# Kernel optimization log

Measured on AMD Instinct MI355X. Metric: run time of the kernel, lower is better.

## Reference

```python
import jax, jax.numpy as jnp
import numpy as np

FEATURE_SIZE = 10 * 64 * 64  # 40960
HIDDEN1 = 512
HIDDEN2 = 256
BATCH = 4096


def setup_inputs() -> dict:
    key = jax.random.key(0)
    ks = jax.random.split(key, 8)
    # Sparse binary-ish features emulated as dense uniform (math is identical).
    white_features = jax.random.uniform(ks[0], (BATCH, FEATURE_SIZE), dtype=jnp.float32)
    black_features = jax.random.uniform(ks[1], (BATCH, FEATURE_SIZE), dtype=jnp.float32)
    s_ft = 1.0 / np.sqrt(FEATURE_SIZE)
    s_fc1 = 1.0 / np.sqrt(HIDDEN1 * 2)
    s_fc2 = 1.0 / np.sqrt(HIDDEN2)
    ft_w = jax.random.uniform(ks[2], (HIDDEN1, FEATURE_SIZE), minval=-s_ft, maxval=s_ft, dtype=jnp.float32)
    ft_b = jax.random.uniform(ks[3], (HIDDEN1,), minval=-s_ft, maxval=s_ft, dtype=jnp.float32)
    fc1_w = jax.random.uniform(ks[4], (HIDDEN2, HIDDEN1 * 2), minval=-s_fc1, maxval=s_fc1, dtype=jnp.float32)
    fc1_b = jax.random.uniform(ks[5], (HIDDEN2,), minval=-s_fc1, maxval=s_fc1, dtype=jnp.float32)
    fc2_w = jax.random.uniform(ks[6], (1, HIDDEN2), minval=-s_fc2, maxval=s_fc2, dtype=jnp.float32)
    fc2_b = jax.random.uniform(ks[7], (1,), minval=-s_fc2, maxval=s_fc2, dtype=jnp.float32)
    return dict(white_features=white_features, black_features=black_features,
                ft_w=ft_w, ft_b=ft_b, fc1_w=fc1_w, fc1_b=fc1_b, fc2_w=fc2_w, fc2_b=fc2_b)


def reference(white_features, black_features, ft_w, ft_b, fc1_w, fc1_b, fc2_w, fc2_b):
    # Feature transform per perspective, clamped to [0, 1]
    white_ft = jnp.clip(white_features @ ft_w.T + ft_b, 0.0, 1.0)  # [B, H1]
    black_ft = jnp.clip(black_features @ ft_w.T + ft_b, 0.0, 1.0)  # [B, H1]
    combined = jnp.concatenate([white_ft, black_ft], axis=1)       # [B, 2*H1]
    x = jax.nn.relu(combined @ fc1_w.T + fc1_b)                    # [B, H2]
    x = x @ fc2_w.T + fc2_b                                        # [B, 1]
    return x.squeeze(-1)
```

## Files before the change

kernel.cpp:

```cpp
#include <hip/hip_runtime.h>
#include <stdint.h>

#define BATCH 4096
#define FEAT  40960
#define H1    512
#define KS    4
#define KCHUNK (FEAT / KS)
#define NSTEPS (KCHUNK / 32)
#define NTILES (FEAT / 32)
#define WTILE  32768

typedef float f32x4 __attribute__((ext_vector_type(4)));
typedef short s16x8 __attribute__((ext_vector_type(8)));
typedef unsigned int u32x2 __attribute__((ext_vector_type(2)));
typedef unsigned int u32x4 __attribute__((ext_vector_type(4)));

__device__ __forceinline__ unsigned bfpack2(float lo, float hi) {
  unsigned a = __float_as_uint(lo);
  unsigned b = __float_as_uint(hi);
  a += 0x7FFFu + ((a >> 16) & 1u);
  b += 0x7FFFu + ((b >> 16) & 1u);
  return (a >> 16) | (b & 0xFFFF0000u);
}

__device__ __forceinline__ int lds_swz(int r, int cb) {
  return (r << 6) + (cb ^ (((r >> 1) & 3) << 4));
}

__global__ __launch_bounds__(512)
void wcvt_kernel(const float* __restrict__ ftw, char* __restrict__ wbf) {
  const int T = blockIdx.x;
  const int tid = threadIdx.x;
  const int c  = tid & 7;
  const int r0 = tid >> 3;
#pragma unroll
  for (int pass = 0; pass < 8; ++pass) {
    const int r = pass * 64 + r0;
    const float* src = ftw + (size_t)r * FEAT + T * 32 + c * 4;
    f32x4 v = *(const f32x4*)src;
    u32x2 o;
    o.x = bfpack2(v.x, v.y);
    o.y = bfpack2(v.z, v.w);
    const int nb = r >> 6, f = (r >> 4) & 3, lr = r & 15;
    const int l = (c >> 1) * 16 + lr;
    *(u32x2*)(wbf + (size_t)T * WTILE + ((nb * 4 + f) << 10) + l * 16 +
              (c & 1) * 8) = o;
  }
}

__global__ __launch_bounds__(512, 4)
void ft_gemm_kernel(const float* __restrict__ whiteF,
                    const float* __restrict__ blackF,
                    const char* __restrict__ wbf,
                    float* __restrict__ Ppart) {
  __shared__ char smem[8192];

  const int tid = threadIdx.x, bid = blockIdx.x;
  const int wgid = (bid & 7) * 64 + (bid >> 3);
  const int ks = wgid >> 7;
  const int p  = (wgid >> 6) & 1;
  const int mt = wgid & 63;

  const float* Ag =
      (p == 0 ? whiteF : blackF) + (size_t)(mt * 64) * FEAT + ks * KCHUNK;

  const int a_row = tid >> 3, a_kc = tid & 7;
  const float* aptr = Ag + (size_t)a_row * FEAT + a_kc * 4;
  const int awoff = lds_swz(a_row, a_kc * 8);

  const int lane = tid & 63, wave = tid >> 6;
  const int lrow = lane & 15, lkb = (lane >> 4) * 16;

  const char* wsrc =
      wbf + (size_t)ks * NSTEPS * WTILE + (wave << 12) + lane * 16;

  int a_off[4];
#pragma unroll
  for (int m = 0; m < 4; ++m) a_off[m] = lds_swz(m * 16 + lrow, lkb);

  f32x4 acc[4][4];
#pragma unroll
  for (int m = 0; m < 4; ++m)
#pragma unroll
    for (int n = 0; n < 4; ++n) acc[m][n] = (f32x4){0.f, 0.f, 0.f, 0.f};

  f32x4 raA;
  u32x4 rb[2][4];

  raA = *(const f32x4*)aptr;
#pragma unroll
  for (int n = 0; n < 4; ++n)
    rb[0][n] = *(const u32x4*)(wsrc + (n << 10));

#define GSTEP(B, LAST, t)                                                     \
  {                                                                           \
                    \
    u32x2 av;                                                                 \
    av.x = bfpack2(raA.x, raA.y);                                             \
    av.y = bfpack2(raA.z, raA.w);                                             \
    *(u32x2*)(smem + (B) * 4096 + awoff) = av;                                \
    if (!(LAST)) {    \
      raA = *(const f32x4*)(aptr + (size_t)((t) + 1) * 32);                   \
                                             \
      const char* wsp = wsrc + (size_t)((t) + 1) * WTILE;                     \
      _Pragma("unroll") for (int n = 0; n < 4; ++n)                           \
          rb[(B) ^ 1][n] = *(const u32x4*)(wsp + (n << 10));                  \
    }                                                                         \
    asm volatile("s_waitcnt lgkmcnt(0)" ::: "memory");   \
    __builtin_amdgcn_sched_barrier(0);                                        \
    __builtin_amdgcn_s_barrier();                                             \
    __builtin_amdgcn_sched_barrier(0);                                        \
    const char* base = smem + (B) * 4096;                                     \
    s16x8 af[4];                                                              \
    _Pragma("unroll") for (int m = 0; m < 4; ++m)                             \
        af[m] = *(const s16x8*)(base + a_off[m]);                             \
    _Pragma("unroll") for (int n = 0; n < 4; ++n) {                           \
      s16x8 bfn = __builtin_bit_cast(s16x8, rb[B][n]);                        \
      _Pragma("unroll") for (int m = 0; m < 4; ++m)                           \
          acc[m][n] = __builtin_amdgcn_mfma_f32_16x16x32_bf16(                \
              af[m], bfn, acc[m][n], 0, 0, 0);                                \
    }                                                                         \
  }

  for (int tt = 0; tt < NSTEPS - 2; tt += 2) {
    GSTEP(0, false, tt);
    GSTEP(1, false, tt + 1);
  }
  GSTEP(0, false, NSTEPS - 2);
  GSTEP(1, true, NSTEPS - 1);
#undef GSTEP

  float* Pp = Ppart + ((size_t)(ks * 2 + p) * BATCH + mt * 64) * H1;
  const int r0 = (lane >> 4) * 4;
  const int c0 = wave * 64 + lrow;
#pragma unroll
  for (int m = 0; m < 4; ++m)
#pragma unroll
    for (int n = 0; n < 4; ++n) {
      float* dst = Pp + (size_t)(r0 + m * 16) * H1 + c0 + n * 16;
#pragma unroll
      for (int j = 0; j < 4; ++j) dst[(size_t)j * H1] = acc[m][n][j];
    }
}

__global__ __launch_bounds__(256)
void ft_reduce_kernel(const float* __restrict__ Ppart,
                      const float* __restrict__ ftb,
                      unsigned short* __restrict__ comb) {
  const size_t gid = (size_t)blockIdx.x * 256 + threadIdx.x;
  const int    pp  = (int)(gid / (BATCH * H1 / 4));
  const size_t rem = gid % (BATCH * H1 / 4);
  const int    row = (int)(rem / (H1 / 4));
  const int    n4  = (int)(rem % (H1 / 4)) * 4;

  f32x4 s = (f32x4){0.f, 0.f, 0.f, 0.f};
#pragma unroll
  for (int ks = 0; ks < KS; ++ks)
    s += *(const f32x4*)(Ppart + ((size_t)(ks * 2 + pp) * BATCH + row) * H1 + n4);
  const f32x4 bv = *(const f32x4*)(ftb + n4);
  s += bv;
  s.x = fminf(fmaxf(s.x, 0.f), 1.f);
  s.y = fminf(fmaxf(s.y, 0.f), 1.f);
  s.z = fminf(fmaxf(s.z, 0.f), 1.f);
  s.w = fminf(fmaxf(s.w, 0.f), 1.f);

  u32x2 o;
  o.x = bfpack2(s.x, s.y);
  o.y = bfpack2(s.z, s.w);
  *(u32x2*)(comb + (size_t)row * 1024 + pp * H1 + n4) = o;
}

__global__ __launch_bounds__(256)
void fc_kernel(const unsigned short* __restrict__ comb,
               const float* __restrict__ w1, const float* __restrict__ b1,
               const float* __restrict__ w2, const float* __restrict__ b2,
               float* __restrict__ out) {
  __shared__ char smem[40960];
  __shared__ float rowsum[64];

  const int tid = threadIdx.x;
  const int bm  = blockIdx.x;
  if (tid < 64) rowsum[tid] = 0.f;

  const int a_row = tid >> 2, a_kq = tid & 3;
  const unsigned short* aptr = comb + (size_t)(bm * 64 + a_row) * 1024 + a_kq * 8;
  const float* wptr = w1 + (size_t)a_row * 1024 + a_kq * 8;

  u32x4 raA;
  f32x4 rw0[4], rw1[4];
  auto issue = [&](int t) {
    raA = *(const u32x4*)(aptr + t * 32);
    const float* wp = wptr + t * 32;
#pragma unroll
    for (int s = 0; s < 4; ++s) {
      rw0[s] = *(const f32x4*)(wp + (size_t)s * 64 * 1024);
      rw1[s] = *(const f32x4*)(wp + (size_t)s * 64 * 1024 + 4);
    }
  };

  const int aoff_w = lds_swz(a_row, a_kq * 16);
  int woff_w[4];
#pragma unroll
  for (int s = 0; s < 4; ++s)
    woff_w[s] = 4096 + lds_swz(s * 64 + a_row, a_kq * 16);

  auto cvtwrite = [&](int b) {
    char* base = smem + b * 20480;
    *(u32x4*)(base + aoff_w) = raA;
#pragma unroll
    for (int s = 0; s < 4; ++s) {
      u32x4 wv;
      wv.x = bfpack2(rw0[s].x, rw0[s].y); wv.y = bfpack2(rw0[s].z, rw0[s].w);
      wv.z = bfpack2(rw1[s].x, rw1[s].y); wv.w = bfpack2(rw1[s].z, rw1[s].w);
      *(u32x4*)(base + woff_w[s]) = wv;
    }
  };

  const int lane = tid & 63, wn = tid >> 6;
  const int lrow = lane & 15, lkb = (lane >> 4) * 16;
  int a_off[4], b_off[4];
#pragma unroll
  for (int m = 0; m < 4; ++m) a_off[m] = lds_swz(m * 16 + lrow, lkb);
#pragma unroll
  for (int n = 0; n < 4; ++n) b_off[n] = 4096 + lds_swz(wn * 64 + n * 16 + lrow, lkb);

  f32x4 acc[4][4];
#pragma unroll
  for (int m = 0; m < 4; ++m)
#pragma unroll
    for (int n = 0; n < 4; ++n) acc[m][n] = (f32x4){0.f, 0.f, 0.f, 0.f};

  issue(0);
  for (int t = 0; t < 32; ++t) {
    const int b = t & 1;
    cvtwrite(b);
    if (t + 1 < 32) issue(t + 1);
    asm volatile("s_waitcnt lgkmcnt(0)" ::: "memory");
    __builtin_amdgcn_sched_barrier(0);
    __builtin_amdgcn_s_barrier();
    __builtin_amdgcn_sched_barrier(0);
    char* base = smem + b * 20480;
    s16x8 af[4];
#pragma unroll
    for (int m = 0; m < 4; ++m) af[m] = *(const s16x8*)(base + a_off[m]);
#pragma unroll
    for (int n = 0; n < 4; ++n) {
      s16x8 bfn = *(const s16x8*)(base + b_off[n]);
#pragma unroll
      for (int m = 0; m < 4; ++m)
        acc[m][n] = __builtin_amdgcn_mfma_f32_16x16x32_bf16(af[m], bfn, acc[m][n], 0, 0, 0);
    }
  }

  float b1v[4], w2v[4];
#pragma unroll
  for (int n = 0; n < 4; ++n) {
    const int col = wn * 64 + n * 16 + lrow;
    b1v[n] = b1[col];
    w2v[n] = w2[col];
  }
#pragma unroll
  for (int m = 0; m < 4; ++m)
#pragma unroll
    for (int j = 0; j < 4; ++j) {
      float v = 0.f;
#pragma unroll
      for (int n = 0; n < 4; ++n) {
        float x = acc[m][n][j] + b1v[n];
        x = fmaxf(x, 0.f);
        v += x * w2v[n];
      }
#pragma unroll
      for (int d = 1; d < 16; d <<= 1) v += __shfl_xor(v, d, 64);
      if ((lane & 15) == 0)
        atomicAdd(&rowsum[m * 16 + (lane >> 4) * 4 + j], v);
    }
  __syncthreads();
  if (tid < 64) {
    out[bm * 64 + tid] = rowsum[tid] + b2[0];
  }
}

extern "C" void kernel_launch(void* const* d_in, const int* in_sizes, int n_in,
                              void* d_out, int out_size, void* d_ws, size_t ws_size,
                              hipStream_t stream) {
  const float* whiteF = (const float*)d_in[0];
  const float* blackF = (const float*)d_in[1];
  const float* ftw    = (const float*)d_in[2];
  const float* ftb    = (const float*)d_in[3];
  const float* w1     = (const float*)d_in[4];
  const float* b1     = (const float*)d_in[5];
  const float* w2     = (const float*)d_in[6];
  const float* b2     = (const float*)d_in[7];

  char* wbf = (char*)d_ws;
  const size_t wbf_bytes   = (size_t)NTILES * WTILE;
  const size_t ppart_bytes = (size_t)KS * 2 * BATCH * H1 * sizeof(float);
  float* Ppart = (float*)((char*)d_ws + wbf_bytes);
  unsigned short* comb = (unsigned short*)((char*)d_ws + wbf_bytes + ppart_bytes);
  float* outp = (float*)d_out;

  hipLaunchKernelGGL(wcvt_kernel, dim3(NTILES), dim3(512), 0, stream, ftw, wbf);
  hipLaunchKernelGGL(ft_gemm_kernel, dim3(512), dim3(512), 0, stream,
                     whiteF, blackF, wbf, Ppart);
  hipLaunchKernelGGL(ft_reduce_kernel, dim3((2 * BATCH * H1 / 4) / 256), dim3(256),
                     0, stream, Ppart, ftb, comb);
  hipLaunchKernelGGL(fc_kernel, dim3(BATCH / 64), dim3(256), 0, stream,
                     comb, w1, b1, w2, b2, outp);
}
```

Before: 553.6 us.

## Stream FT weight tiles into LDS via global_load_lds with two-deep prefetch

Weight tiles for the feature-transform GEMM are now copied straight from global memory into double-buffered LDS slots with global_load_lds, instead of being held in registers. Activations are prefetched two steps ahead through vmcnt-based waits. The aim is to free VGPRs and hide global-load latency behind the MFMA work. The LDS footprint grows from 8 KB to 72 KB per 512-thread block, which conflicts with the launch_bounds occupancy hint of 4 blocks and likely cuts resident blocks per CU. The hand-counted vmcnt values also have to match the exact load order.

```diff
diff --git a/kernel.cpp b/kernel.cpp
--- a/kernel.cpp
+++ b/kernel.cpp
@@ -9,6 +9,8 @@
 #define NSTEPS (KCHUNK / 32)
 #define NTILES (FEAT / 32)
 #define WTILE  32768
+#define WSLOT  32768
+#define ALDS   65536
 
 typedef float f32x4 __attribute__((ext_vector_type(4)));
 typedef short s16x8 __attribute__((ext_vector_type(8)));
@@ -25,6 +27,12 @@
 
 __device__ __forceinline__ int lds_swz(int r, int cb) {
   return (r << 6) + (cb ^ (((r >> 1) & 3) << 4));
+}
+
+__device__ __forceinline__ void glds16(const void* g, void* l) {
+  __builtin_amdgcn_global_load_lds(
+      (const __attribute__((address_space(1))) unsigned*)g,
+      (__attribute__((address_space(3))) unsigned*)l, 16, 0, 0);
 }
 
 __global__ __launch_bounds__(512)
@@ -53,7 +61,7 @@
                     const float* __restrict__ blackF,
                     const char* __restrict__ wbf,
                     float* __restrict__ Ppart) {
-  __shared__ char smem[8192];
+  __shared__ char smem[73728];
 
   const int tid = threadIdx.x, bid = blockIdx.x;
   const int wgid = (bid & 7) * 64 + (bid >> 3);
@@ -73,6 +81,7 @@
 
   const char* wsrc =
       wbf + (size_t)ks * NSTEPS * WTILE + (wave << 12) + lane * 16;
+  const int wofs = (wave << 12);
 
   int a_off[4];
 #pragma unroll
@@ -84,51 +93,76 @@
 #pragma unroll
     for (int n = 0; n < 4; ++n) acc[m][n] = (f32x4){0.f, 0.f, 0.f, 0.f};
 
-  f32x4 raA;
-  u32x4 rb[2][4];
-
-  raA = *(const f32x4*)aptr;
-#pragma unroll
-  for (int n = 0; n < 4; ++n)
-    rb[0][n] = *(const u32x4*)(wsrc + (n << 10));
-
-#define GSTEP(B, LAST, t)                                                     \
+  f32x4 raA[2];
+
+  raA[0] = *(const f32x4*)aptr;
+  raA[1] = *(const f32x4*)(aptr + 32);
+#pragma unroll
+  for (int c = 0; c < 4; ++c)
+    glds16(wsrc + c * 1024, smem + 0 * WSLOT + wofs + c * 1024);
+#pragma unroll
+  for (int c = 0; c < 4; ++c)
+    glds16(wsrc + WTILE + c * 1024, smem + 1 * WSLOT + wofs + c * 1024);
+  asm volatile("s_waitcnt vmcnt(9)" ::: "memory");
+  __builtin_amdgcn_sched_barrier(0);
+  {
+    u32x2 av;
+    av.x = bfpack2(raA[0].x, raA[0].y);
+    av.y = bfpack2(raA[0].z, raA[0].w);
+    *(u32x2*)(smem + ALDS + 0 * 4096 + awoff) = av;
+  }
+  raA[0] = *(const f32x4*)(aptr + 2 * 32);
+  asm volatile("s_waitcnt lgkmcnt(0)" ::: "memory");
+  __builtin_amdgcn_sched_barrier(0);
+  __builtin_amdgcn_s_barrier();
+  __builtin_amdgcn_sched_barrier(0);
+
+#define GSTEP(B, t)                                                           \
   {                                                                           \
-                    \
-    u32x2 av;                                                                 \
-    av.x = bfpack2(raA.x, raA.y);                                             \
-    av.y = bfpack2(raA.z, raA.w);                                             \
-    *(u32x2*)(smem + (B) * 4096 + awoff) = av;                                \
-    if (!(LAST)) {    \
-      raA = *(const f32x4*)(aptr + (size_t)((t) + 1) * 32);                   \
-                                             \
-      const char* wsp = wsrc + (size_t)((t) + 1) * WTILE;                     \
-      _Pragma("unroll") for (int n = 0; n < 4; ++n)                           \
-          rb[(B) ^ 1][n] = *(const u32x4*)(wsp + (n << 10));                  \
+    asm volatile("s_waitcnt vmcnt(5)" ::: "memory");   \
+    __builtin_amdgcn_sched_barrier(0);                                        \
+    const char* wbase = smem + (B) * WSLOT + wofs;                            \
+    const char* abase = smem + ALDS + (B) * 4096;                             \
+    s16x8 af[4], wb[4];                                                       \
+    _Pragma("unroll") for (int m = 0; m < 4; ++m)                             \
+        af[m] = *(const s16x8*)(abase + a_off[m]);                            \
+    _Pragma("unroll") for (int n = 0; n < 4; ++n)                             \
+        wb[n] = *(const s16x8*)(wbase + n * 1024 + lane * 16);                \
+    asm volatile("s_waitcnt lgkmcnt(0)" ::: "memory");      \
+    __builtin_amdgcn_sched_barrier(0);                                        \
+    {                     \
+      const int t2 = ((t) + 2 < NSTEPS) ? (t) + 2 : NSTEPS - 1;               \
+      const char* wsp = wsrc + (size_t)t2 * WTILE;                            \
+      char* wdp = smem + (B) * WSLOT + wofs;                                  \
+      _Pragma("unroll") for (int c = 0; c < 4; ++c)                           \
+          glds16(wsp + c * 1024, wdp + c * 1024);                             \
     }                                                                         \
+    {        \
+      u32x2 av;                                                               \
+      av.x = bfpack2(raA[(B) ^ 1].x, raA[(B) ^ 1].y);                         \
+      av.y = bfpack2(raA[(B) ^ 1].z, raA[(B) ^ 1].w);                         \
+      *(u32x2*)(smem + ALDS + ((B) ^ 1) * 4096 + awoff) = av;                 \
+      const int t3 = ((t) + 3 < NSTEPS) ? (t) + 3 : NSTEPS - 1;               \
+      raA[(B) ^ 1] = *(const f32x4*)(aptr + (size_t)t3 * 32);                 \
+    }                                                                         \
+    _Pragma("unroll") for (int n = 0; n < 4; ++n)                             \
+      _Pragma("unroll") for (int m = 0; m < 4; ++m)                           \
+          acc[m][n] = __builtin_amdgcn_mfma_f32_16x16x32_bf16(                \
+              af[m], wb[n], acc[m][n], 0, 0, 0);                              \
     asm volatile("s_waitcnt lgkmcnt(0)" ::: "memory");   \
     __builtin_amdgcn_sched_barrier(0);                                        \
     __builtin_amdgcn_s_barrier();                                             \
     __builtin_amdgcn_sched_barrier(0);                                        \
-    const char* base = smem + (B) * 4096;                                     \
-    s16x8 af[4];                                                              \
-    _Pragma("unroll") for (int m = 0; m < 4; ++m)                             \
-        af[m] = *(const s16x8*)(base + a_off[m]);                             \
-    _Pragma("unroll") for (int n = 0; n < 4; ++n) {                           \
-      s16x8 bfn = __builtin_bit_cast(s16x8, rb[B][n]);                        \
-      _Pragma("unroll") for (int m = 0; m < 4; ++m)                           \
-          acc[m][n] = __builtin_amdgcn_mfma_f32_16x16x32_bf16(                \
-              af[m], bfn, acc[m][n], 0, 0, 0);                                \
-    }                                                                         \
-  }
-
-  for (int tt = 0; tt < NSTEPS - 2; tt += 2) {
-    GSTEP(0, false, tt);
-    GSTEP(1, false, tt + 1);
-  }
-  GSTEP(0, false, NSTEPS - 2);
-  GSTEP(1, true, NSTEPS - 1);
+  }
+
+  for (int tt = 0; tt < NSTEPS; tt += 2) {
+    GSTEP(0, tt);
+    GSTEP(1, tt + 1);
+  }
 #undef GSTEP
+
+  asm volatile("s_waitcnt vmcnt(0) lgkmcnt(0)" ::: "memory");
+  __builtin_amdgcn_sched_barrier(0);
 
   float* Pp = Ppart + ((size_t)(ks * 2 + p) * BATCH + mt * 64) * H1;
   const int r0 = (lane >> 4) * 4;
```

Result: faster. 541.6 us (-2.2%).

## Stream fp32 A tiles directly to LDS via global_load_lds with macro-step pipeline

Applied to the files above, without the earlier changes.

Replaces the register-staged A path (global load, bf16 pack, LDS store each 32-wide step) with direct global-to-LDS async loads of fp32 A tiles covering 128 K per macro step, double-buffered in 64KB of LDS. The bf16 conversion moves to after the LDS read using the hardware v_cvt_pk_bf16_f32 instruction. Barriers drop from one per 32-K step to one per 128-K step, and B weight loads are interleaved across micro-steps. The cost is much larger LDS use, which can limit occupancy below the 4-blocks-per-CU launch bound, plus extra conversion work per wave since each wave converts A fragments redundantly.

```diff
diff --git a/kernel.cpp b/kernel.cpp
--- a/kernel.cpp
+++ b/kernel.cpp
@@ -7,6 +7,7 @@
 #define KS    4
 #define KCHUNK (FEAT / KS)
 #define NSTEPS (KCHUNK / 32)
+#define NMACRO (KCHUNK / 128)
 #define NTILES (FEAT / 32)
 #define WTILE  32768
 
@@ -23,9 +24,23 @@
   return (a >> 16) | (b & 0xFFFF0000u);
 }
 
+__device__ __forceinline__ unsigned cvtpk(float lo, float hi) {
+  unsigned r;
+  asm("v_cvt_pk_bf16_f32 %0, %1, %2" : "=v"(r) : "v"(lo), "v"(hi));
+  return r;
+}
+
 __device__ __forceinline__ int lds_swz(int r, int cb) {
   return (r << 6) + (cb ^ (((r >> 1) & 3) << 4));
 }
+
+__device__ __forceinline__ void glds16(const void* g, void* l) {
+  __builtin_amdgcn_global_load_lds(
+      (const __attribute__((address_space(1))) unsigned*)g,
+      (__attribute__((address_space(3))) unsigned*)l, 16, 0, 0);
+}
+
+#define SFENCE() __builtin_amdgcn_sched_barrier(0)
 
 __global__ __launch_bounds__(512)
 void wcvt_kernel(const float* __restrict__ ftw, char* __restrict__ wbf) {
@@ -53,7 +68,7 @@
                     const float* __restrict__ blackF,
                     const char* __restrict__ wbf,
                     float* __restrict__ Ppart) {
-  __shared__ char smem[8192];
+  __shared__ char smem[65536];
 
   const int tid = threadIdx.x, bid = blockIdx.x;
   const int wgid = (bid & 7) * 64 + (bid >> 3);
@@ -63,20 +78,30 @@
 
   const float* Ag =
       (p == 0 ? whiteF : blackF) + (size_t)(mt * 64) * FEAT + ks * KCHUNK;
-
-  const int a_row = tid >> 3, a_kc = tid & 7;
-  const float* aptr = Ag + (size_t)a_row * FEAT + a_kc * 4;
-  const int awoff = lds_swz(a_row, a_kc * 8);
+  const char* Agc = (const char*)Ag;
 
   const int lane = tid & 63, wave = tid >> 6;
-  const int lrow = lane & 15, lkb = (lane >> 4) * 16;
-
-  const char* wsrc =
-      wbf + (size_t)ks * NSTEPS * WTILE + (wave << 12) + lane * 16;
-
-  int a_off[4];
-#pragma unroll
-  for (int m = 0; m < 4; ++m) a_off[m] = lds_swz(m * 16 + lrow, lkb);
+  const int lrow = lane & 15, lkq = lane >> 4;
+
+  unsigned aoff[4];
+  int adst[4];
+  const int c31 = lane & 31;
+#pragma unroll
+  for (int j = 0; j < 4; ++j) {
+    const int rr = wave * 8 + 2 * j + (lane >> 5);
+    aoff[j] = (unsigned)rr * (FEAT * 4u) + (unsigned)((c31 ^ (rr & 7)) << 4);
+    adst[j] = (wave * 8 + 2 * j) * 512;
+  }
+
+  int adA[4][2];
+#pragma unroll
+  for (int m = 0; m < 4; ++m)
+#pragma unroll
+    for (int i = 0; i < 2; ++i)
+      adA[m][i] = (m * 16 + lrow) * 512 + ((((lkq << 1) | i) ^ (lrow & 7)) << 4);
+
+  const char* wptr =
+      wbf + (size_t)(ks * NSTEPS) * WTILE + (wave << 12) + lane * 16;
 
   f32x4 acc[4][4];
 #pragma unroll
@@ -84,54 +109,75 @@
 #pragma unroll
     for (int n = 0; n < 4; ++n) acc[m][n] = (f32x4){0.f, 0.f, 0.f, 0.f};
 
-  f32x4 raA;
-  u32x4 rb[2][4];
-
-  raA = *(const f32x4*)aptr;
-#pragma unroll
-  for (int n = 0; n < 4; ++n)
-    rb[0][n] = *(const u32x4*)(wsrc + (n << 10));
-
-#define GSTEP(B, LAST, t)                                                     \
+  u32x4 wb[4];
+
+#pragma unroll
+  for (int j = 0; j < 4; ++j) glds16(Agc + aoff[j], smem + adst[j]);
+  SFENCE();
+#pragma unroll
+  for (int n = 0; n < 4; ++n) wb[n] = *(const u32x4*)(wptr + (n << 10));
+#pragma unroll
+  for (int j = 0; j < 4; ++j) aoff[j] += 512;
+  asm volatile("s_waitcnt vmcnt(4)" ::: "memory");
+  SFENCE();
+  __builtin_amdgcn_s_barrier();
+  SFENCE();
+
+#define MICRO(B, JM, T)                                                       \
   {                                                                           \
-                    \
-    u32x2 av;                                                                 \
-    av.x = bfpack2(raA.x, raA.y);                                             \
-    av.y = bfpack2(raA.z, raA.w);                                             \
-    *(u32x2*)(smem + (B) * 4096 + awoff) = av;                                \
-    if (!(LAST)) {    \
-      raA = *(const f32x4*)(aptr + (size_t)((t) + 1) * 32);                   \
-                                             \
-      const char* wsp = wsrc + (size_t)((t) + 1) * WTILE;                     \
-      _Pragma("unroll") for (int n = 0; n < 4; ++n)                           \
-          rb[(B) ^ 1][n] = *(const u32x4*)(wsp + (n << 10));                  \
+    s16x8 af[4];                                                              \
+    _Pragma("unroll") for (int m = 0; m < 4; ++m) {                           \
+      f32x4 lo = *(const f32x4*)(smem + adA[m][0] + (B) * 32768 + (JM) * 128);\
+      f32x4 hi = *(const f32x4*)(smem + adA[m][1] + (B) * 32768 + (JM) * 128);\
+      u32x4 cv;                                                               \
+      cv.x = cvtpk(lo.x, lo.y); cv.y = cvtpk(lo.z, lo.w);                     \
+      cv.z = cvtpk(hi.x, hi.y); cv.w = cvtpk(hi.z, hi.w);                     \
+      af[m] = __builtin_bit_cast(s16x8, cv);                                  \
     }                                                                         \
-    asm volatile("s_waitcnt lgkmcnt(0)" ::: "memory");   \
-    __builtin_amdgcn_sched_barrier(0);                                        \
-    __builtin_amdgcn_s_barrier();                                             \
-    __builtin_amdgcn_sched_barrier(0);                                        \
-    const char* base = smem + (B) * 4096;                                     \
-    s16x8 af[4];                                                              \
-    _Pragma("unroll") for (int m = 0; m < 4; ++m)                             \
-        af[m] = *(const s16x8*)(base + a_off[m]);                             \
-    _Pragma("unroll") for (int n = 0; n < 4; ++n) {                           \
-      s16x8 bfn = __builtin_bit_cast(s16x8, rb[B][n]);                        \
+    _Pragma("unroll") for (int n = 0; n < 4; ++n)                             \
       _Pragma("unroll") for (int m = 0; m < 4; ++m)                           \
           acc[m][n] = __builtin_amdgcn_mfma_f32_16x16x32_bf16(                \
-              af[m], bfn, acc[m][n], 0, 0, 0);                                \
+              af[m], __builtin_bit_cast(s16x8, wb[n]), acc[m][n], 0, 0, 0);   \
+    if ((JM) < 3) {            \
+      const char* wsp = wptr + (size_t)(4 * (T) + (JM) + 1) * WTILE;          \
+      _Pragma("unroll") for (int n = 0; n < 4; ++n)                           \
+          wb[n] = *(const u32x4*)(wsp + (n << 10));                           \
+      glds16(Agc + aoff[JM], smem + (((B) ^ 1) * 32768) + adst[JM]);          \
+    } else {        \
+      glds16(Agc + aoff[3], smem + (((B) ^ 1) * 32768) + adst[3]);            \
+      SFENCE();                                                               \
+      const char* wsp = wptr + (size_t)(4 * (T) + 4) * WTILE;                 \
+      _Pragma("unroll") for (int n = 0; n < 4; ++n)                           \
+          wb[n] = *(const u32x4*)(wsp + (n << 10));                           \
     }                                                                         \
   }
 
-  for (int tt = 0; tt < NSTEPS - 2; tt += 2) {
-    GSTEP(0, false, tt);
-    GSTEP(1, false, tt + 1);
-  }
-  GSTEP(0, false, NSTEPS - 2);
-  GSTEP(1, true, NSTEPS - 1);
-#undef GSTEP
+#define MACRO(B, T)                                                           \
+  {                                                                           \
+    MICRO(B, 0, T);                                                           \
+    MICRO(B, 1, T);                                                           \
+    MICRO(B, 2, T);                                                           \
+    MICRO(B, 3, T);                                                           \
+    asm volatile("s_waitcnt vmcnt(4)" ::: "memory");        \
+    SFENCE();                                                                 \
+    __builtin_amdgcn_s_barrier();                                             \
+    SFENCE();                                                                 \
+    const unsigned adv = ((T) + 2 < NMACRO) ? 512u : 0u;                      \
+    _Pragma("unroll") for (int j = 0; j < 4; ++j) aoff[j] += adv;             \
+  }
+
+  for (int TT = 0; TT < NMACRO; TT += 2) {
+    MACRO(0, TT);
+    MACRO(1, TT + 1);
+  }
+#undef MACRO
+#undef MICRO
+
+  asm volatile("s_waitcnt vmcnt(0) lgkmcnt(0)" ::: "memory");
+  SFENCE();
 
   float* Pp = Ppart + ((size_t)(ks * 2 + p) * BATCH + mt * 64) * H1;
-  const int r0 = (lane >> 4) * 4;
+  const int r0 = lkq * 4;
   const int c0 = wave * 64 + lrow;
 #pragma unroll
   for (int m = 0; m < 4; ++m)
```

Result: slower. 638.2 us (+15.3%).

## Enlarge FT GEMM tile to 128 rows with 64-wide K steps

Applied to the files above, without the earlier changes.

The feature-transform GEMM now uses 1024-thread workgroups covering 128 batch rows, so each bf16 weight tile read from global memory serves twice as many rows and weight traffic per output drops. Each iteration processes a 64-wide K chunk as two 32-wide halves in a 32KB double-buffered LDS area, which halves the number of barriers. The global A loads, weight prefetch and bf16 packing are reordered so they overlap the MFMA work. The cost is fewer workgroups (256), more LDS and registers per block, and possibly lower occupancy.

```diff
diff --git a/kernel.cpp b/kernel.cpp
--- a/kernel.cpp
+++ b/kernel.cpp
@@ -7,6 +7,7 @@
 #define KS    4
 #define KCHUNK (FEAT / KS)
 #define NSTEPS (KCHUNK / 32)
+#define NSTEP64 (KCHUNK / 64)
 #define NTILES (FEAT / 32)
 #define WTILE  32768
 
@@ -48,35 +49,37 @@
   }
 }
 
-__global__ __launch_bounds__(512, 4)
+__global__ __launch_bounds__(1024, 4)
 void ft_gemm_kernel(const float* __restrict__ whiteF,
                     const float* __restrict__ blackF,
                     const char* __restrict__ wbf,
                     float* __restrict__ Ppart) {
-  __shared__ char smem[8192];
+  __shared__ char smem[32768];
 
   const int tid = threadIdx.x, bid = blockIdx.x;
-  const int wgid = (bid & 7) * 64 + (bid >> 3);
-  const int ks = wgid >> 7;
-  const int p  = (wgid >> 6) & 1;
-  const int mt = wgid & 63;
+  const int wgid = (bid & 7) * 32 + (bid >> 3);
+  const int ks = wgid >> 6;
+  const int p  = (wgid >> 5) & 1;
+  const int mt = wgid & 31;
 
   const float* Ag =
-      (p == 0 ? whiteF : blackF) + (size_t)(mt * 64) * FEAT + ks * KCHUNK;
-
-  const int a_row = tid >> 3, a_kc = tid & 7;
-  const float* aptr = Ag + (size_t)a_row * FEAT + a_kc * 4;
-  const int awoff = lds_swz(a_row, a_kc * 8);
+      (p == 0 ? whiteF : blackF) + (size_t)(mt * 128) * FEAT + ks * KCHUNK;
+
+  const int a_row = tid >> 3, a_oct = tid & 7;
+  const float* aptr = Ag + (size_t)a_row * FEAT + a_oct * 8;
+  const int awoff = (a_oct >> 2) * 8192 + lds_swz(a_row, (a_oct & 3) * 16);
 
   const int lane = tid & 63, wave = tid >> 6;
-  const int lrow = lane & 15, lkb = (lane >> 4) * 16;
+  const int wm = wave >> 3, wn = wave & 7;
+  const int lrow = lane & 15, lkq = lane >> 4;
 
   const char* wsrc =
-      wbf + (size_t)ks * NSTEPS * WTILE + (wave << 12) + lane * 16;
+      wbf + (size_t)(ks * NSTEPS) * WTILE + (wn << 12) + lane * 16;
 
   int a_off[4];
 #pragma unroll
-  for (int m = 0; m < 4; ++m) a_off[m] = lds_swz(m * 16 + lrow, lkb);
+  for (int m = 0; m < 4; ++m)
+    a_off[m] = lds_swz(wm * 64 + m * 16 + lrow, lkq * 16);
 
   f32x4 acc[4][4];
 #pragma unroll
@@ -84,55 +87,84 @@
 #pragma unroll
     for (int n = 0; n < 4; ++n) acc[m][n] = (f32x4){0.f, 0.f, 0.f, 0.f};
 
-  f32x4 raA;
-  u32x4 rb[2][4];
-
-  raA = *(const f32x4*)aptr;
-#pragma unroll
-  for (int n = 0; n < 4; ++n)
-    rb[0][n] = *(const u32x4*)(wsrc + (n << 10));
-
-#define GSTEP(B, LAST, t)                                                     \
+  f32x4 raA0, raA1;
+  u32x4 wb[4];
+
+  raA0 = *(const f32x4*)aptr;
+  raA1 = *(const f32x4*)(aptr + 4);
+#pragma unroll
+  for (int n = 0; n < 4; ++n) wb[n] = *(const u32x4*)(wsrc + (n << 10));
+  {
+    u32x4 av;
+    av.x = bfpack2(raA0.x, raA0.y); av.y = bfpack2(raA0.z, raA0.w);
+    av.z = bfpack2(raA1.x, raA1.y); av.w = bfpack2(raA1.z, raA1.w);
+    *(u32x4*)(smem + awoff) = av;
+  }
+  raA0 = *(const f32x4*)(aptr + 64);
+  raA1 = *(const f32x4*)(aptr + 68);
+  asm volatile("s_waitcnt lgkmcnt(0)" ::: "memory");
+  __builtin_amdgcn_sched_barrier(0);
+  __builtin_amdgcn_s_barrier();
+  __builtin_amdgcn_sched_barrier(0);
+
+#define GSTEP(B, t)                                                           \
   {                                                                           \
-                    \
-    u32x2 av;                                                                 \
-    av.x = bfpack2(raA.x, raA.y);                                             \
-    av.y = bfpack2(raA.z, raA.w);                                             \
-    *(u32x2*)(smem + (B) * 4096 + awoff) = av;                                \
-    if (!(LAST)) {    \
-      raA = *(const f32x4*)(aptr + (size_t)((t) + 1) * 32);                   \
-                                             \
-      const char* wsp = wsrc + (size_t)((t) + 1) * WTILE;                     \
+    const char* abase = smem + (B) * 16384;                                   \
+    s16x8 af[4];                                                              \
+                                       \
+    _Pragma("unroll") for (int m = 0; m < 4; ++m)                             \
+        af[m] = *(const s16x8*)(abase + a_off[m]);                            \
+    _Pragma("unroll") for (int n = 0; n < 4; ++n)                             \
+      _Pragma("unroll") for (int m = 0; m < 4; ++m)                           \
+          acc[m][n] = __builtin_amdgcn_mfma_f32_16x16x32_bf16(                \
+              af[m], __builtin_bit_cast(s16x8, wb[n]), acc[m][n], 0, 0, 0);   \
+    {                          \
+      const char* wsp = wsrc + (size_t)(2 * (t) + 1) * WTILE;                 \
       _Pragma("unroll") for (int n = 0; n < 4; ++n)                           \
-          rb[(B) ^ 1][n] = *(const u32x4*)(wsp + (n << 10));                  \
+          wb[n] = *(const u32x4*)(wsp + (n << 10));                           \
     }                                                                         \
-    asm volatile("s_waitcnt lgkmcnt(0)" ::: "memory");   \
+    {        \
+      u32x4 av;                                                               \
+      av.x = bfpack2(raA0.x, raA0.y); av.y = bfpack2(raA0.z, raA0.w);         \
+      av.z = bfpack2(raA1.x, raA1.y); av.w = bfpack2(raA1.z, raA1.w);         \
+      *(u32x4*)(smem + ((B) ^ 1) * 16384 + awoff) = av;                       \
+    }                                                                         \
+    {                                                       \
+      const int t2 = ((t) + 2 < NSTEP64) ? (t) + 2 : NSTEP64 - 1;             \
+      raA0 = *(const f32x4*)(aptr + (size_t)t2 * 64);                         \
+      raA1 = *(const f32x4*)(aptr + (size_t)t2 * 64 + 4);                     \
+    }                                                                         \
+                \
+    _Pragma("unroll") for (int m = 0; m < 4; ++m)                             \
+        af[m] = *(const s16x8*)(abase + 8192 + a_off[m]);                     \
+    _Pragma("unroll") for (int n = 0; n < 4; ++n)                             \
+      _Pragma("unroll") for (int m = 0; m < 4; ++m)                           \
+          acc[m][n] = __builtin_amdgcn_mfma_f32_16x16x32_bf16(                \
+              af[m], __builtin_bit_cast(s16x8, wb[n]), acc[m][n], 0, 0, 0);   \
+    {                                             \
+      const int t1 = ((t) + 1 < NSTEP64) ? (t) + 1 : NSTEP64 - 1;             \
+      const char* wsp = wsrc + (size_t)(2 * t1) * WTILE;                      \
+      _Pragma("unroll") for (int n = 0; n < 4; ++n)                           \
+          wb[n] = *(const u32x4*)(wsp + (n << 10));                           \
+    }                                                                         \
+    asm volatile("s_waitcnt lgkmcnt(0)" ::: "memory");                        \
     __builtin_amdgcn_sched_barrier(0);                                        \
     __builtin_amdgcn_s_barrier();                                             \
     __builtin_amdgcn_sched_barrier(0);                                        \
-    const char* base = smem + (B) * 4096;                                     \
-    s16x8 af[4];                                                              \
-    _Pragma("unroll") for (int m = 0; m < 4; ++m)                             \
-        af[m] = *(const s16x8*)(base + a_off[m]);                             \
-    _Pragma("unroll") for (int n = 0; n < 4; ++n) {                           \
-      s16x8 bfn = __builtin_bit_cast(s16x8, rb[B][n]);                        \
-      _Pragma("unroll") for (int m = 0; m < 4; ++m)                           \
-          acc[m][n] = __builtin_amdgcn_mfma_f32_16x16x32_bf16(                \
-              af[m], bfn, acc[m][n], 0, 0, 0);                                \
-    }                                                                         \
-  }
-
-  for (int tt = 0; tt < NSTEPS - 2; tt += 2) {
-    GSTEP(0, false, tt);
-    GSTEP(1, false, tt + 1);
-  }
-  GSTEP(0, false, NSTEPS - 2);
-  GSTEP(1, true, NSTEPS - 1);
+  }
+
+  for (int tt = 0; tt < NSTEP64; tt += 2) {
+    GSTEP(0, tt);
+    GSTEP(1, tt + 1);
+  }
 #undef GSTEP
 
-  float* Pp = Ppart + ((size_t)(ks * 2 + p) * BATCH + mt * 64) * H1;
-  const int r0 = (lane >> 4) * 4;
-  const int c0 = wave * 64 + lrow;
+  asm volatile("s_waitcnt vmcnt(0) lgkmcnt(0)" ::: "memory");
+  __builtin_amdgcn_sched_barrier(0);
+
+  float* Pp = Ppart + ((size_t)(ks * 2 + p) * BATCH + mt * 128) * H1;
+  const int r0 = wm * 64 + lkq * 4;
+  const int c0 = wn * 64 + lrow;
 #pragma unroll
   for (int m = 0; m < 4; ++m)
 #pragma unroll
@@ -301,7 +333,7 @@
   float* outp = (float*)d_out;
 
   hipLaunchKernelGGL(wcvt_kernel, dim3(NTILES), dim3(512), 0, stream, ftw, wbf);
-  hipLaunchKernelGGL(ft_gemm_kernel, dim3(512), dim3(512), 0, stream,
+  hipLaunchKernelGGL(ft_gemm_kernel, dim3(256), dim3(1024), 0, stream,
                      whiteF, blackF, wbf, Ppart);
   hipLaunchKernelGGL(ft_reduce_kernel, dim3((2 * BATCH * H1 / 4) / 256), dim3(256),
                      0, stream, Ppart, ftb, comb);
```

Result: slower. 712.5 us (+28.7%).
